# Optimization experiments

Measured on AMD Instinct MI355X. Metric: run time of the kernel, lower is better.

Reference implementation:

```python
import jax, jax.numpy as jnp
import numpy as np

N = 50000      # nodes
E = 800000     # edges
IN = 256       # in_dim
D = 64         # hidden_dim per head
H = 4          # heads
OUT = 40       # out_dim (classes)
SLOPE = 0.2    # leaky relu negative slope


def _gat_conv(h, src, dst, W, al, ar, heads, dh, res=None, act=False):
    """DGL-style GATConv. h:[N,Fin], W:[Fin,heads*dh], al/ar:[heads,dh]."""
    n = h.shape[0]
    feat = (h @ W).reshape(n, heads, dh)                 # [N,H,D]
    el = jnp.sum(feat * al, axis=-1)                     # [N,H]
    er = jnp.sum(feat * ar, axis=-1)                     # [N,H]
    e = jax.nn.leaky_relu(el[src] + er[dst], SLOPE)      # [E,H]
    # segment softmax over incoming edges of each dst node
    m = jax.ops.segment_max(e, dst, num_segments=n)      # [N,H]
    ex = jnp.exp(e - m[dst])                             # [E,H]
    s = jax.ops.segment_sum(ex, dst, num_segments=n)     # [N,H]
    alpha = ex / s[dst]                                  # [E,H]
    rst = jax.ops.segment_sum(alpha[:, :, None] * feat[src], dst, num_segments=n)  # [N,H,D]
    if res is not None:
        rst = rst + res
    if act:
        rst = jax.nn.elu(rst)
    return rst


def setup_inputs():
    key = jax.random.key(0)
    ks = jax.random.split(key, 16)
    def p(k, shape, fan_in):
        return (jax.random.normal(k, shape, jnp.float32) / np.sqrt(fan_in)).astype(jnp.float32)
    inputs = jax.random.normal(ks[0], (N, IN), jnp.float32)
    src = jax.random.randint(ks[1], (E,), 0, N, dtype=jnp.int32)
    dst = jax.random.randint(ks[2], (E,), 0, N, dtype=jnp.int32)
    return {
        "inputs": inputs, "src": src, "dst": dst,
        "W0": p(ks[3], (IN, H * D), IN), "al0": p(ks[4], (H, D), D), "ar0": p(ks[5], (H, D), D),
        "W1": p(ks[6], (H * D, H * D), H * D), "al1": p(ks[7], (H, D), D), "ar1": p(ks[8], (H, D), D),
        "Wo": p(ks[9], (H * D, H * OUT), H * D), "alo": p(ks[10], (H, OUT), OUT), "aro": p(ks[11], (H, OUT), OUT),
        "res_Wo": p(ks[12], (H * D, H * OUT), H * D),
        "fc_W": p(ks[13], (IN, D), IN),
    }


def reference(inputs, src, dst, W0, al0, ar0, W1, al1, ar1, Wo, alo, aro, res_Wo, fc_W):
    # layer 0: no residual, elu activation
    h = _gat_conv(inputs, src, dst, W0, al0, ar0, H, D, res=None, act=True)
    h = h.reshape(N, H * D)
    # layer 1: identity residual (in_feats == heads*out_feats), elu
    res1 = h.reshape(N, H, D)
    h = _gat_conv(h, src, dst, W1, al1, ar1, H, D, res=res1, act=True)
    h = h.reshape(N, H * D)
    # output layer: linear residual projection, no activation, mean over heads
    res_o = (h @ res_Wo).reshape(N, H, OUT)
    logits = _gat_conv(h, src, dst, Wo, alo, aro, H, OUT, res=res_o, act=False).mean(axis=1)
    seq_fts = inputs @ fc_W
    return (logits, h, seq_fts)
```

## Files before the change

### kernel.cpp

```cpp
#include <hip/hip_runtime.h>

typedef unsigned short u16;
typedef unsigned int u32;
typedef __attribute__((ext_vector_type(8))) short short8;
typedef __attribute__((ext_vector_type(4))) float f32x4;

#define NN 50000
#define EE 800000

__device__ __forceinline__ float b2f(u16 u){ union{float f;u32 i;}x; x.i=((u32)u)<<16; return x.f; }
__device__ __forceinline__ u16 f2b(float f){ union{float f;u32 i;}x; x.f=f; u32 i=x.i; return (u16)((i + 0x7fffu + ((i>>16)&1u))>>16); }

__global__ void k_f2b4(const float* __restrict__ x, u16* __restrict__ y, int n4){
  int i = blockIdx.x*256 + threadIdx.x;
  if (i >= n4) return;
  float4 v = ((const float4*)x)[i];
  ushort4 o; o.x=f2b(v.x); o.y=f2b(v.y); o.z=f2b(v.z); o.w=f2b(v.w);
  ((ushort4*)y)[i]=o;
}

__global__ void k_catWo(const float* __restrict__ rWo, const float* __restrict__ Wo, u16* __restrict__ Bcat){
  int i = blockIdx.x*256 + threadIdx.x;
  if (i >= 256*320) return;
  int k = i/320, c = i%320;
  float v = (c < 160) ? rWo[k*160 + c] : Wo[k*160 + (c-160)];
  Bcat[i] = f2b(v);
}

__global__ void k_count(const int* __restrict__ dst, int* __restrict__ cnt){
  int i = blockIdx.x*256+threadIdx.x; if (i<EE) atomicAdd(&cnt[dst[i]],1);
}

__global__ void k_scan_blocks(const int* __restrict__ cnt, int* __restrict__ off, int* __restrict__ part, int n){
  __shared__ int ts[256];
  int t = threadIdx.x; int base = blockIdx.x*1024 + t*4;
  int c0 = (base+0<n)?cnt[base+0]:0;
  int c1 = (base+1<n)?cnt[base+1]:0;
  int c2 = (base+2<n)?cnt[base+2]:0;
  int c3 = (base+3<n)?cnt[base+3]:0;
  int s = c0+c1+c2+c3;
  ts[t]=s; __syncthreads();
  for (int d=1; d<256; d<<=1){ int v=(t>=d)?ts[t-d]:0; __syncthreads(); ts[t]+=v; __syncthreads(); }
  int ex = ts[t]-s;
  if (t==255) part[blockIdx.x]=ts[255];
  if (base+0<n) off[base+0]=ex; ex+=c0;
  if (base+1<n) off[base+1]=ex; ex+=c1;
  if (base+2<n) off[base+2]=ex; ex+=c2;
  if (base+3<n) off[base+3]=ex;
}

__global__ void k_scan_part(int* part, int nb){
  if (threadIdx.x==0 && blockIdx.x==0){ int run=0; for(int i=0;i<nb;++i){ int v=part[i]; part[i]=run; run+=v; } }
}

__global__ void k_addback(int* off, const int* __restrict__ part, int n){
  int base = blockIdx.x*1024 + threadIdx.x*4; int p = part[blockIdx.x];
  #pragma unroll
  for (int j=0;j<4;++j) if (base+j<n) off[base+j]+=p;
}

__global__ void k_copy(const int* __restrict__ a, int* __restrict__ b, int n){
  int i=blockIdx.x*256+threadIdx.x; if(i<n) b[i]=a[i];
}

__global__ void k_scatter(const int* __restrict__ src, const int* __restrict__ dst, int* __restrict__ cur,
                          int* __restrict__ srcs){
  int i = blockIdx.x*256+threadIdx.x; if (i>=EE) return;
  int d = dst[i]; int p = atomicAdd(&cur[d],1);
  srcs[p]=src[i];
}

template<int MODE>
__global__ __launch_bounds__(256) void k_gemm(const u16* __restrict__ A, const u16* __restrict__ B,
                                              void* __restrict__ C0, void* __restrict__ C1,
                                              int M, int N){
  __shared__ u16 Bt[64][266];
  const int tid = threadIdx.x;
  const int n0 = blockIdx.y * 64;
  const int row0 = blockIdx.x * 256;
  #pragma unroll
  for (int r=0; r<32; ++r){
    int lin = r*256 + tid;
    int kk = lin >> 5;
    int cp = (lin & 31) << 1;
    ushort2 v = *(const ushort2*)(B + (size_t)kk*N + n0 + cp);
    Bt[cp][kk] = v.x; Bt[cp+1][kk] = v.y;
  }
  __syncthreads();
  const int w = tid >> 6, l = tid & 63;
  const int lr = l & 15, lq = l >> 4;
  const int wrow = row0 + w*64;
  f32x4 acc[4][4];
  #pragma unroll
  for (int fr=0; fr<4; ++fr)
    #pragma unroll
    for (int j=0; j<4; ++j) acc[fr][j] = (f32x4)0.0f;
  #pragma unroll
  for (int k0 = 0; k0 < 256; k0 += 32){
    short8 a[4], b[4];
    #pragma unroll
    for (int fr=0; fr<4; ++fr){
      int r = wrow + fr*16 + lr; r = r < M ? r : M-1;
      a[fr] = *(const short8*)(A + (size_t)r*256 + k0 + lq*8);
    }
    #pragma unroll
    for (int j=0; j<4; ++j)
      b[j] = *(const short8*)(&Bt[j*16 + lr][k0 + lq*8]);
    #pragma unroll
    for (int fr=0; fr<4; ++fr)
      #pragma unroll
      for (int j=0; j<4; ++j)
        acc[fr][j] = __builtin_amdgcn_mfma_f32_16x16x32_bf16(a[fr], b[j], acc[fr][j], 0, 0, 0);
  }
  #pragma unroll
  for (int fr=0; fr<4; ++fr)
    #pragma unroll
    for (int j=0; j<4; ++j)
      #pragma unroll
      for (int q=0; q<4; ++q){
        int r = wrow + fr*16 + lq*4 + q;
        if (r < M){
          int c = n0 + j*16 + lr;
          float v = acc[fr][j][q];
          if constexpr (MODE == 0)      ((float*)C0)[(size_t)r*N + c] = v;
          else if constexpr (MODE == 1) ((u16*)C0)[(size_t)r*N + c] = f2b(v);
          else {
            if (c < 160) ((u16*)C0)[(size_t)r*160 + c]       = f2b(v);
            else         ((u16*)C1)[(size_t)r*160 + (c-160)] = f2b(v);
          }
        }
      }
}

__global__ void k_eler(const u16* __restrict__ feat, const float* __restrict__ al, const float* __restrict__ ar,
                       float* __restrict__ el, float* __restrict__ er, int Dh, int HD){
  int t = blockIdx.x*256 + threadIdx.x;
  int n = t >> 6; int l = t & 63;
  if (n >= NN) return;
  int h = l >> 4, s = l & 15;
  const u16* fr = feat + (size_t)n*HD + h*Dh;
  const float* alh = al + h*Dh; const float* arh = ar + h*Dh;
  float accl = 0.f, accr = 0.f;
  for (int d = s; d < Dh; d += 16){ float f = b2f(fr[d]); accl += f*alh[d]; accr += f*arh[d]; }
  #pragma unroll
  for (int m = 8; m >= 1; m >>= 1){ accl += __shfl_xor(accl, m, 64); accr += __shfl_xor(accr, m, 64); }
  if (s == 0){ el[n*4+h] = accl; er[n*4+h] = accr; }
}

__global__ void k_soft(const float* __restrict__ el, const float* __restrict__ er,
                       const int* __restrict__ srcs, const int* __restrict__ off,
                       float* __restrict__ es, float* __restrict__ recs){
  int n = blockIdx.x*256 + threadIdx.x; if (n >= NN) return;
  int o0 = off[n], o1 = off[n+1];
  float4 e4 = ((const float4*)er)[n];
  float4 m; m.x=m.y=m.z=m.w=-1e30f;
  for (int i=o0;i<o1;++i){
    float4 a = ((const float4*)el)[srcs[i]];
    float vx=a.x+e4.x; vx = vx>=0.f?vx:0.2f*vx;
    float vy=a.y+e4.y; vy = vy>=0.f?vy:0.2f*vy;
    float vz=a.z+e4.z; vz = vz>=0.f?vz:0.2f*vz;
    float vw=a.w+e4.w; vw = vw>=0.f?vw:0.2f*vw;
    m.x=fmaxf(m.x,vx); m.y=fmaxf(m.y,vy); m.z=fmaxf(m.z,vz); m.w=fmaxf(m.w,vw);
  }
  float4 s; s.x=s.y=s.z=s.w=0.f;
  for (int i=o0;i<o1;++i){
    float4 a = ((const float4*)el)[srcs[i]];
    float vx=a.x+e4.x; vx = vx>=0.f?vx:0.2f*vx;
    float vy=a.y+e4.y; vy = vy>=0.f?vy:0.2f*vy;
    float vz=a.z+e4.z; vz = vz>=0.f?vz:0.2f*vz;
    float vw=a.w+e4.w; vw = vw>=0.f?vw:0.2f*vw;
    float4 v;
    v.x=__expf(vx-m.x); v.y=__expf(vy-m.y); v.z=__expf(vz-m.z); v.w=__expf(vw-m.w);
    ((float4*)es)[i]=v; s.x+=v.x; s.y+=v.y; s.z+=v.z; s.w+=v.w;
  }
  float4 r;
  r.x = s.x>0.f ? 1.f/s.x : 0.f;
  r.y = s.y>0.f ? 1.f/s.y : 0.f;
  r.z = s.z>0.f ? 1.f/s.z : 0.f;
  r.w = s.w>0.f ? 1.f/s.w : 0.f;
  ((float4*)recs)[n] = r;
}

template<bool RES>
__global__ __launch_bounds__(256) void k_agg64(const u16* __restrict__ feat, const float* __restrict__ es,
    const float* __restrict__ recs, const int* __restrict__ off, const int* __restrict__ srcs,
    const u16* __restrict__ resid, float* __restrict__ outf, u16* __restrict__ outb){
  int l = threadIdx.x & 63, w = threadIdx.x >> 6;
  int n = blockIdx.x*4 + w;
  int o0 = off[n], o1 = off[n+1];
  int h = l >> 4;
  float ax=0.f, ay=0.f, az=0.f, aw=0.f;
  int i = o0;
  for (; i + 4 <= o1; i += 4){
    int s0 = srcs[i], s1 = srcs[i+1], s2 = srcs[i+2], s3 = srcs[i+3];
    float e0 = es[(size_t)i*4 + h],     e1 = es[(size_t)(i+1)*4 + h];
    float e2 = es[(size_t)(i+2)*4 + h], e3 = es[(size_t)(i+3)*4 + h];
    ushort4 f0 = *(const ushort4*)(feat + (size_t)s0*256 + l*4);
    ushort4 f1 = *(const ushort4*)(feat + (size_t)s1*256 + l*4);
    ushort4 f2 = *(const ushort4*)(feat + (size_t)s2*256 + l*4);
    ushort4 f3 = *(const ushort4*)(feat + (size_t)s3*256 + l*4);
    ax += e0*b2f(f0.x) + e1*b2f(f1.x) + e2*b2f(f2.x) + e3*b2f(f3.x);
    ay += e0*b2f(f0.y) + e1*b2f(f1.y) + e2*b2f(f2.y) + e3*b2f(f3.y);
    az += e0*b2f(f0.z) + e1*b2f(f1.z) + e2*b2f(f2.z) + e3*b2f(f3.z);
    aw += e0*b2f(f0.w) + e1*b2f(f1.w) + e2*b2f(f2.w) + e3*b2f(f3.w);
  }
  for (; i < o1; ++i){
    int s0 = srcs[i];
    float e0 = es[(size_t)i*4 + h];
    ushort4 f0 = *(const ushort4*)(feat + (size_t)s0*256 + l*4);
    ax += e0*b2f(f0.x); ay += e0*b2f(f0.y); az += e0*b2f(f0.z); aw += e0*b2f(f0.w);
  }
  float rc = recs[n*4+h];
  float vx = ax*rc, vy = ay*rc, vz = az*rc, vw = aw*rc;
  if (RES){
    ushort4 r4 = *(const ushort4*)(resid + (size_t)n*256 + l*4);
    vx += b2f(r4.x); vy += b2f(r4.y); vz += b2f(r4.z); vw += b2f(r4.w);
  }
  vx = vx > 0.f ? vx : expm1f(vx);
  vy = vy > 0.f ? vy : expm1f(vy);
  vz = vz > 0.f ? vz : expm1f(vz);
  vw = vw > 0.f ? vw : expm1f(vw);
  if (outf){ float4 v; v.x=vx; v.y=vy; v.z=vz; v.w=vw; *(float4*)(outf + (size_t)n*256 + l*4) = v; }
  ushort4 ob; ob.x=f2b(vx); ob.y=f2b(vy); ob.z=f2b(vz); ob.w=f2b(vw);
  *(ushort4*)(outb + (size_t)n*256 + l*4) = ob;
}

__global__ __launch_bounds__(256) void k_agg_out(const u16* __restrict__ feat, const float* __restrict__ es,
    const float* __restrict__ recs, const int* __restrict__ off, const int* __restrict__ srcs,
    const u16* __restrict__ reso, float* __restrict__ logits){
  __shared__ float2 red[4][4][80];
  __shared__ float fin[4][160];
  const int l = threadIdx.x & 63, w = threadIdx.x >> 6;
  const int n = blockIdx.x*4 + w;
  const int o0 = off[n], o1 = off[n+1];
  int sArr[5], dpArr[5], hArr[5];
  #pragma unroll
  for (int r=0;r<5;++r){
    int p = r*64 + l;
    sArr[r] = p/80; dpArr[r] = p%80; hArr[r] = dpArr[r]/20;
  }
  float2 acc[5];
  #pragma unroll
  for (int r=0;r<5;++r){ acc[r].x=0.f; acc[r].y=0.f; }
  for (int i0 = o0; i0 < o1; i0 += 4){
    int cnt = o1 - i0;
    #pragma unroll
    for (int r=0;r<5;++r){
      int s = sArr[r];
      bool valid = s < cnt;
      int e = valid ? (i0 + s) : i0;
      int sv = srcs[e];
      float al = es[(size_t)e*4 + hArr[r]];
      ushort2 f = *(const ushort2*)(feat + (size_t)sv*160 + dpArr[r]*2);
      if (!valid) al = 0.f;
      acc[r].x += al * b2f(f.x);
      acc[r].y += al * b2f(f.y);
    }
  }
  #pragma unroll
  for (int r=0;r<5;++r) red[w][sArr[r]][dpArr[r]] = acc[r];
  __syncthreads();
  float4 rc = ((const float4*)recs)[n];
  const float* rcp = (const float*)&rc;
  {
    int dp = l;
    float vx = red[w][0][dp].x + red[w][1][dp].x + red[w][2][dp].x + red[w][3][dp].x;
    float vy = red[w][0][dp].y + red[w][1][dp].y + red[w][2][dp].y + red[w][3][dp].y;
    float r0 = rcp[dp/20];
    ushort2 rr = *(const ushort2*)(reso + (size_t)n*160 + dp*2);
    fin[w][dp*2]   = vx*r0 + b2f(rr.x);
    fin[w][dp*2+1] = vy*r0 + b2f(rr.y);
  }
  if (l < 16){
    int dp = 64 + l;
    float vx = red[w][0][dp].x + red[w][1][dp].x + red[w][2][dp].x + red[w][3][dp].x;
    float vy = red[w][0][dp].y + red[w][1][dp].y + red[w][2][dp].y + red[w][3][dp].y;
    float r0 = rcp[3];
    ushort2 rr = *(const ushort2*)(reso + (size_t)n*160 + dp*2);
    fin[w][dp*2]   = vx*r0 + b2f(rr.x);
    fin[w][dp*2+1] = vy*r0 + b2f(rr.y);
  }
  __syncthreads();
  if (l < 40) logits[(size_t)n*40 + l] = 0.25f*(fin[w][l]+fin[w][l+40]+fin[w][l+80]+fin[w][l+120]);
}

extern "C" void kernel_launch(void* const* d_in, const int* in_sizes, int n_in,
                              void* d_out, int out_size, void* d_ws, size_t ws_size,
                              hipStream_t stream){
  const float* inputs = (const float*)d_in[0];
  const int*   src    = (const int*)d_in[1];
  const int*   dst    = (const int*)d_in[2];
  const float* W0  = (const float*)d_in[3];
  const float* al0 = (const float*)d_in[4];
  const float* ar0 = (const float*)d_in[5];
  const float* W1  = (const float*)d_in[6];
  const float* al1 = (const float*)d_in[7];
  const float* ar1 = (const float*)d_in[8];
  const float* Wo  = (const float*)d_in[9];
  const float* alo = (const float*)d_in[10];
  const float* aro = (const float*)d_in[11];
  const float* rWo = (const float*)d_in[12];
  const float* fcW = (const float*)d_in[13];

  float* out = (float*)d_out;
  float* out_logits = out;
  float* out_h      = out + 2000000;
  float* out_seq    = out + 14800000;

  char* ws = (char*)d_ws;
  size_t o = 0;
  auto alc = [&](size_t bytes){ size_t r = o; o += (bytes + 255) & ~(size_t)255; return r; };
  size_t oXb   = alc((size_t)NN*256*2);
  size_t oFA   = alc((size_t)NN*256*2);
  size_t oFB   = alc((size_t)NN*256*2);
  size_t oEs   = alc((size_t)EE*4*4);
  size_t oSrcs = alc((size_t)EE*4);
  size_t oOff  = alc((size_t)(NN+1)*4);
  size_t oCnt  = alc((size_t)(NN+1)*4);
  size_t oCur  = alc((size_t)NN*4);
  size_t oPart = alc(64*4);
  size_t oEl   = alc((size_t)NN*4*4);
  size_t oEr   = alc((size_t)NN*4*4);
  size_t oRecs = alc((size_t)NN*4*4);
  size_t oReso = alc((size_t)NN*160*2);
  size_t oW0b  = alc(256*256*2);
  size_t oW1b  = alc(256*256*2);
  size_t oWcat = alc(256*320*2);
  size_t oFcb  = alc(256*64*2);
  if (ws_size < o) return;

  u16* Xb   = (u16*)(ws + oXb);
  u16* fA   = (u16*)(ws + oFA);
  u16* fB   = (u16*)(ws + oFB);
  float* es = (float*)(ws + oEs);
  int* srcs = (int*)(ws + oSrcs);
  int* off  = (int*)(ws + oOff);
  int* cnt  = (int*)(ws + oCnt);
  int* cur  = (int*)(ws + oCur);
  int* part = (int*)(ws + oPart);
  float* el = (float*)(ws + oEl);
  float* er = (float*)(ws + oEr);
  float* recs = (float*)(ws + oRecs);
  u16* reso = (u16*)(ws + oReso);
  u16* W0b  = (u16*)(ws + oW0b);
  u16* W1b  = (u16*)(ws + oW1b);
  u16* Wcat = (u16*)(ws + oWcat);
  u16* fcb  = (u16*)(ws + oFcb);

  k_f2b4<<<(NN*256/4 + 255)/256, 256, 0, stream>>>(inputs, Xb, NN*256/4);
  k_f2b4<<<(65536/4 + 255)/256, 256, 0, stream>>>(W0, W0b, 65536/4);
  k_f2b4<<<(65536/4 + 255)/256, 256, 0, stream>>>(W1, W1b, 65536/4);
  k_catWo<<<(256*320 + 255)/256, 256, 0, stream>>>(rWo, Wo, Wcat);
  k_f2b4<<<(16384/4 + 255)/256, 256, 0, stream>>>(fcW, fcb, 16384/4);

  hipMemsetAsync(cnt, 0, (size_t)(NN+1)*4, stream);
  k_count<<<(EE+255)/256, 256, 0, stream>>>(dst, cnt);
  const int NP1 = NN+1, NB = (NP1 + 1023)/1024;
  k_scan_blocks<<<NB, 256, 0, stream>>>(cnt, off, part, NP1);
  k_scan_part<<<1, 64, 0, stream>>>(part, NB);
  k_addback<<<NB, 256, 0, stream>>>(off, part, NP1);
  k_copy<<<(NN+255)/256, 256, 0, stream>>>(off, cur, NN);
  k_scatter<<<(EE+255)/256, 256, 0, stream>>>(src, dst, cur, srcs);

  dim3 gN256((NN+255)/256, 4), gN320((NN+255)/256, 5), gN64((NN+255)/256, 1);

  k_gemm<0><<<gN64, 256, 0, stream>>>(Xb, fcb, out_seq, nullptr, NN, 64);

  k_gemm<1><<<gN256, 256, 0, stream>>>(Xb, W0b, fA, nullptr, NN, 256);
  k_eler<<<(NN*64 + 255)/256, 256, 0, stream>>>(fA, al0, ar0, el, er, 64, 256);
  k_soft<<<(NN+255)/256, 256, 0, stream>>>(el, er, srcs, off, es, recs);
  k_agg64<false><<<NN/4, 256, 0, stream>>>(fA, es, recs, off, srcs, nullptr, nullptr, fB);

  k_gemm<1><<<gN256, 256, 0, stream>>>(fB, W1b, fA, nullptr, NN, 256);
  k_eler<<<(NN*64 + 255)/256, 256, 0, stream>>>(fA, al1, ar1, el, er, 64, 256);
  k_soft<<<(NN+255)/256, 256, 0, stream>>>(el, er, srcs, off, es, recs);
  k_agg64<true><<<NN/4, 256, 0, stream>>>(fA, es, recs, off, srcs, fB, out_h, fB);

  k_gemm<2><<<gN320, 256, 0, stream>>>(fB, Wcat, reso, fA, NN, 320);
  k_eler<<<(NN*64 + 255)/256, 256, 0, stream>>>(fA, alo, aro, el, er, 40, 160);
  k_soft<<<(NN+255)/256, 256, 0, stream>>>(el, er, srcs, off, es, recs);
  k_agg_out<<<NN/4, 256, 0, stream>>>(fA, es, recs, off, srcs, reso, out_logits);
}
```

Baseline: 566.5 us.

## Widen gather loads in aggregation kernels and cache leaky-relu scores in softmax

The 64-dim aggregation now has each half-wavefront handle a different edge, with 16-byte bf16 loads per lane, and combines the two halves with a cross-lane shuffle. The output-layer aggregation switches to 8-byte loads and 8 edges per iteration, reducing through a larger shared-memory buffer. The softmax kernel stores the leaky-relu scores during the max pass and rereads them, so it no longer gathers el[src] a second time. A specialized el/er kernel for 256-wide features uses vectorized loads of features and attention weights. Risks are extra writes to es, idle half-wavefronts during the epilogue, and tail-edge masking overhead on low-degree nodes.

```diff
diff --git a/kernel.cpp b/kernel.cpp
--- a/kernel.cpp
+++ b/kernel.cpp
@@ -132,6 +132,23 @@
       }
 }
 
+__global__ void k_eler256(const u16* __restrict__ feat, const float* __restrict__ al, const float* __restrict__ ar,
+                          float* __restrict__ el, float* __restrict__ er){
+  int t = blockIdx.x*256 + threadIdx.x;
+  int n = t >> 6, l = t & 63;
+  if (n >= NN) return;
+  float4 a4 = ((const float4*)al)[l];
+  float4 r4 = ((const float4*)ar)[l];
+  ushort4 f = *(const ushort4*)(feat + (size_t)n*256 + l*4);
+  float f0=b2f(f.x), f1=b2f(f.y), f2=b2f(f.z), f3=b2f(f.w);
+  float accl = f0*a4.x + f1*a4.y + f2*a4.z + f3*a4.w;
+  float accr = f0*r4.x + f1*r4.y + f2*r4.z + f3*r4.w;
+  #pragma unroll
+  for (int m = 8; m >= 1; m >>= 1){ accl += __shfl_xor(accl, m, 64); accr += __shfl_xor(accr, m, 64); }
+  int h = l >> 4;
+  if ((l & 15) == 0){ el[n*4+h] = accl; er[n*4+h] = accr; }
+}
+
 __global__ void k_eler(const u16* __restrict__ feat, const float* __restrict__ al, const float* __restrict__ ar,
                        float* __restrict__ el, float* __restrict__ er, int Dh, int HD){
   int t = blockIdx.x*256 + threadIdx.x;
@@ -156,21 +173,18 @@
   float4 m; m.x=m.y=m.z=m.w=-1e30f;
   for (int i=o0;i<o1;++i){
     float4 a = ((const float4*)el)[srcs[i]];
-    float vx=a.x+e4.x; vx = vx>=0.f?vx:0.2f*vx;
-    float vy=a.y+e4.y; vy = vy>=0.f?vy:0.2f*vy;
-    float vz=a.z+e4.z; vz = vz>=0.f?vz:0.2f*vz;
-    float vw=a.w+e4.w; vw = vw>=0.f?vw:0.2f*vw;
-    m.x=fmaxf(m.x,vx); m.y=fmaxf(m.y,vy); m.z=fmaxf(m.z,vz); m.w=fmaxf(m.w,vw);
+    float4 v;
+    v.x=a.x+e4.x; v.x = v.x>=0.f?v.x:0.2f*v.x;
+    v.y=a.y+e4.y; v.y = v.y>=0.f?v.y:0.2f*v.y;
+    v.z=a.z+e4.z; v.z = v.z>=0.f?v.z:0.2f*v.z;
+    v.w=a.w+e4.w; v.w = v.w>=0.f?v.w:0.2f*v.w;
+    ((float4*)es)[i]=v;
+    m.x=fmaxf(m.x,v.x); m.y=fmaxf(m.y,v.y); m.z=fmaxf(m.z,v.z); m.w=fmaxf(m.w,v.w);
   }
   float4 s; s.x=s.y=s.z=s.w=0.f;
   for (int i=o0;i<o1;++i){
-    float4 a = ((const float4*)el)[srcs[i]];
-    float vx=a.x+e4.x; vx = vx>=0.f?vx:0.2f*vx;
-    float vy=a.y+e4.y; vy = vy>=0.f?vy:0.2f*vy;
-    float vz=a.z+e4.z; vz = vz>=0.f?vz:0.2f*vz;
-    float vw=a.w+e4.w; vw = vw>=0.f?vw:0.2f*vw;
-    float4 v;
-    v.x=__expf(vx-m.x); v.y=__expf(vy-m.y); v.z=__expf(vz-m.z); v.w=__expf(vw-m.w);
+    float4 v = ((const float4*)es)[i];
+    v.x=__expf(v.x-m.x); v.y=__expf(v.y-m.y); v.z=__expf(v.z-m.z); v.w=__expf(v.w-m.w);
     ((float4*)es)[i]=v; s.x+=v.x; s.y+=v.y; s.z+=v.z; s.w+=v.w;
   }
   float4 r;
@@ -185,100 +199,113 @@
 __global__ __launch_bounds__(256) void k_agg64(const u16* __restrict__ feat, const float* __restrict__ es,
     const float* __restrict__ recs, const int* __restrict__ off, const int* __restrict__ srcs,
     const u16* __restrict__ resid, float* __restrict__ outf, u16* __restrict__ outb){
-  int l = threadIdx.x & 63, w = threadIdx.x >> 6;
-  int n = blockIdx.x*4 + w;
-  int o0 = off[n], o1 = off[n+1];
-  int h = l >> 4;
-  float ax=0.f, ay=0.f, az=0.f, aw=0.f;
+  const int l = threadIdx.x & 63, w = threadIdx.x >> 6;
+  const int n = blockIdx.x*4 + w;
+  const int o0 = off[n], o1 = off[n+1];
+  const int lh = l & 31;
+  const int half = l >> 5;
+  const int h = lh >> 3;
+  float a0=0.f,a1=0.f,a2=0.f,a3=0.f,a4=0.f,a5=0.f,a6=0.f,a7=0.f;
   int i = o0;
-  for (; i + 4 <= o1; i += 4){
-    int s0 = srcs[i], s1 = srcs[i+1], s2 = srcs[i+2], s3 = srcs[i+3];
-    float e0 = es[(size_t)i*4 + h],     e1 = es[(size_t)(i+1)*4 + h];
-    float e2 = es[(size_t)(i+2)*4 + h], e3 = es[(size_t)(i+3)*4 + h];
-    ushort4 f0 = *(const ushort4*)(feat + (size_t)s0*256 + l*4);
-    ushort4 f1 = *(const ushort4*)(feat + (size_t)s1*256 + l*4);
-    ushort4 f2 = *(const ushort4*)(feat + (size_t)s2*256 + l*4);
-    ushort4 f3 = *(const ushort4*)(feat + (size_t)s3*256 + l*4);
-    ax += e0*b2f(f0.x) + e1*b2f(f1.x) + e2*b2f(f2.x) + e3*b2f(f3.x);
-    ay += e0*b2f(f0.y) + e1*b2f(f1.y) + e2*b2f(f2.y) + e3*b2f(f3.y);
-    az += e0*b2f(f0.z) + e1*b2f(f1.z) + e2*b2f(f2.z) + e3*b2f(f3.z);
-    aw += e0*b2f(f0.w) + e1*b2f(f1.w) + e2*b2f(f2.w) + e3*b2f(f3.w);
-  }
-  for (; i < o1; ++i){
-    int s0 = srcs[i];
-    float e0 = es[(size_t)i*4 + h];
-    ushort4 f0 = *(const ushort4*)(feat + (size_t)s0*256 + l*4);
-    ax += e0*b2f(f0.x); ay += e0*b2f(f0.y); az += e0*b2f(f0.z); aw += e0*b2f(f0.w);
-  }
-  float rc = recs[n*4+h];
-  float vx = ax*rc, vy = ay*rc, vz = az*rc, vw = aw*rc;
-  if (RES){
-    ushort4 r4 = *(const ushort4*)(resid + (size_t)n*256 + l*4);
-    vx += b2f(r4.x); vy += b2f(r4.y); vz += b2f(r4.z); vw += b2f(r4.w);
-  }
-  vx = vx > 0.f ? vx : expm1f(vx);
-  vy = vy > 0.f ? vy : expm1f(vy);
-  vz = vz > 0.f ? vz : expm1f(vz);
-  vw = vw > 0.f ? vw : expm1f(vw);
-  if (outf){ float4 v; v.x=vx; v.y=vy; v.z=vz; v.w=vw; *(float4*)(outf + (size_t)n*256 + l*4) = v; }
-  ushort4 ob; ob.x=f2b(vx); ob.y=f2b(vy); ob.z=f2b(vz); ob.w=f2b(vw);
-  *(ushort4*)(outb + (size_t)n*256 + l*4) = ob;
+  for (; i + 8 <= o1; i += 8){
+    #pragma unroll
+    for (int u=0; u<4; ++u){
+      int e = i + u*2 + half;
+      int sv = srcs[e];
+      float al = es[(size_t)e*4 + h];
+      short8 f = *(const short8*)(feat + (size_t)sv*256 + lh*8);
+      a0 += al*b2f((u16)f[0]); a1 += al*b2f((u16)f[1]);
+      a2 += al*b2f((u16)f[2]); a3 += al*b2f((u16)f[3]);
+      a4 += al*b2f((u16)f[4]); a5 += al*b2f((u16)f[5]);
+      a6 += al*b2f((u16)f[6]); a7 += al*b2f((u16)f[7]);
+    }
+  }
+  for (; i < o1; i += 2){
+    int e = i + half;
+    bool valid = e < o1;
+    int ec = valid ? e : i;
+    int sv = srcs[ec];
+    float al = valid ? es[(size_t)ec*4 + h] : 0.f;
+    short8 f = *(const short8*)(feat + (size_t)sv*256 + lh*8);
+    a0 += al*b2f((u16)f[0]); a1 += al*b2f((u16)f[1]);
+    a2 += al*b2f((u16)f[2]); a3 += al*b2f((u16)f[3]);
+    a4 += al*b2f((u16)f[4]); a5 += al*b2f((u16)f[5]);
+    a6 += al*b2f((u16)f[6]); a7 += al*b2f((u16)f[7]);
+  }
+  a0 += __shfl_xor(a0,32,64); a1 += __shfl_xor(a1,32,64);
+  a2 += __shfl_xor(a2,32,64); a3 += __shfl_xor(a3,32,64);
+  a4 += __shfl_xor(a4,32,64); a5 += __shfl_xor(a5,32,64);
+  a6 += __shfl_xor(a6,32,64); a7 += __shfl_xor(a7,32,64);
+  if (half == 0){
+    float rc = recs[n*4+h];
+    float v[8] = {a0*rc,a1*rc,a2*rc,a3*rc,a4*rc,a5*rc,a6*rc,a7*rc};
+    if (RES){
+      short8 r8 = *(const short8*)(resid + (size_t)n*256 + lh*8);
+      #pragma unroll
+      for (int j=0;j<8;++j) v[j] += b2f((u16)r8[j]);
+    }
+    #pragma unroll
+    for (int j=0;j<8;++j) v[j] = v[j] > 0.f ? v[j] : expm1f(v[j]);
+    if (outf){
+      float4 q0; q0.x=v[0]; q0.y=v[1]; q0.z=v[2]; q0.w=v[3];
+      float4 q1; q1.x=v[4]; q1.y=v[5]; q1.z=v[6]; q1.w=v[7];
+      *(float4*)(outf + (size_t)n*256 + lh*8)     = q0;
+      *(float4*)(outf + (size_t)n*256 + lh*8 + 4) = q1;
+    }
+    short8 ob;
+    #pragma unroll
+    for (int j=0;j<8;++j) ob[j] = (short)f2b(v[j]);
+    *(short8*)(outb + (size_t)n*256 + lh*8) = ob;
+  }
 }
 
 __global__ __launch_bounds__(256) void k_agg_out(const u16* __restrict__ feat, const float* __restrict__ es,
     const float* __restrict__ recs, const int* __restrict__ off, const int* __restrict__ srcs,
     const u16* __restrict__ reso, float* __restrict__ logits){
-  __shared__ float2 red[4][4][80];
+  __shared__ f32x4 red[4][8][40];
   __shared__ float fin[4][160];
   const int l = threadIdx.x & 63, w = threadIdx.x >> 6;
   const int n = blockIdx.x*4 + w;
   const int o0 = off[n], o1 = off[n+1];
-  int sArr[5], dpArr[5], hArr[5];
+  int sA[5], qA[5], hA[5];
   #pragma unroll
   for (int r=0;r<5;++r){
     int p = r*64 + l;
-    sArr[r] = p/80; dpArr[r] = p%80; hArr[r] = dpArr[r]/20;
-  }
-  float2 acc[5];
-  #pragma unroll
-  for (int r=0;r<5;++r){ acc[r].x=0.f; acc[r].y=0.f; }
-  for (int i0 = o0; i0 < o1; i0 += 4){
+    sA[r] = p/40; qA[r] = p%40; hA[r] = qA[r]/10;
+  }
+  f32x4 acc[5];
+  #pragma unroll
+  for (int r=0;r<5;++r) acc[r] = (f32x4)0.0f;
+  for (int i0 = o0; i0 < o1; i0 += 8){
     int cnt = o1 - i0;
     #pragma unroll
     for (int r=0;r<5;++r){
-      int s = sArr[r];
+      int s = sA[r];
       bool valid = s < cnt;
       int e = valid ? (i0 + s) : i0;
       int sv = srcs[e];
-      float al = es[(size_t)e*4 + hArr[r]];
-      ushort2 f = *(const ushort2*)(feat + (size_t)sv*160 + dpArr[r]*2);
+      float al = es[(size_t)e*4 + hA[r]];
+      ushort4 f = *(const ushort4*)(feat + (size_t)sv*160 + qA[r]*4);
       if (!valid) al = 0.f;
-      acc[r].x += al * b2f(f.x);
-      acc[r].y += al * b2f(f.y);
+      acc[r][0] += al*b2f(f.x); acc[r][1] += al*b2f(f.y);
+      acc[r][2] += al*b2f(f.z); acc[r][3] += al*b2f(f.w);
     }
   }
   #pragma unroll
-  for (int r=0;r<5;++r) red[w][sArr[r]][dpArr[r]] = acc[r];
+  for (int r=0;r<5;++r) red[w][sA[r]][qA[r]] = acc[r];
   __syncthreads();
-  float4 rc = ((const float4*)recs)[n];
-  const float* rcp = (const float*)&rc;
-  {
-    int dp = l;
-    float vx = red[w][0][dp].x + red[w][1][dp].x + red[w][2][dp].x + red[w][3][dp].x;
-    float vy = red[w][0][dp].y + red[w][1][dp].y + red[w][2][dp].y + red[w][3][dp].y;
-    float r0 = rcp[dp/20];
-    ushort2 rr = *(const ushort2*)(reso + (size_t)n*160 + dp*2);
-    fin[w][dp*2]   = vx*r0 + b2f(rr.x);
-    fin[w][dp*2+1] = vy*r0 + b2f(rr.y);
-  }
-  if (l < 16){
-    int dp = 64 + l;
-    float vx = red[w][0][dp].x + red[w][1][dp].x + red[w][2][dp].x + red[w][3][dp].x;
-    float vy = red[w][0][dp].y + red[w][1][dp].y + red[w][2][dp].y + red[w][3][dp].y;
-    float r0 = rcp[3];
-    ushort2 rr = *(const ushort2*)(reso + (size_t)n*160 + dp*2);
-    fin[w][dp*2]   = vx*r0 + b2f(rr.x);
-    fin[w][dp*2+1] = vy*r0 + b2f(rr.y);
+  if (l < 40){
+    f32x4 v = red[w][0][l];
+    #pragma unroll
+    for (int s=1;s<8;++s) v += red[w][s][l];
+    float4 rc = ((const float4*)recs)[n];
+    const float* rcp = (const float*)&rc;
+    float rch = rcp[l/10];
+    ushort4 rr = *(const ushort4*)(reso + (size_t)n*160 + l*4);
+    fin[w][l*4+0] = v[0]*rch + b2f(rr.x);
+    fin[w][l*4+1] = v[1]*rch + b2f(rr.y);
+    fin[w][l*4+2] = v[2]*rch + b2f(rr.z);
+    fin[w][l*4+3] = v[3]*rch + b2f(rr.w);
   }
   __syncthreads();
   if (l < 40) logits[(size_t)n*40 + l] = 0.25f*(fin[w][l]+fin[w][l+40]+fin[w][l+80]+fin[w][l+120]);
@@ -367,12 +394,12 @@
   k_gemm<0><<<gN64, 256, 0, stream>>>(Xb, fcb, out_seq, nullptr, NN, 64);
 
   k_gemm<1><<<gN256, 256, 0, stream>>>(Xb, W0b, fA, nullptr, NN, 256);
-  k_eler<<<(NN*64 + 255)/256, 256, 0, stream>>>(fA, al0, ar0, el, er, 64, 256);
+  k_eler256<<<(NN*64 + 255)/256, 256, 0, stream>>>(fA, al0, ar0, el, er);
   k_soft<<<(NN+255)/256, 256, 0, stream>>>(el, er, srcs, off, es, recs);
   k_agg64<false><<<NN/4, 256, 0, stream>>>(fA, es, recs, off, srcs, nullptr, nullptr, fB);
 
   k_gemm<1><<<gN256, 256, 0, stream>>>(fB, W1b, fA, nullptr, NN, 256);
-  k_eler<<<(NN*64 + 255)/256, 256, 0, stream>>>(fA, al1, ar1, el, er, 64, 256);
+  k_eler256<<<(NN*64 + 255)/256, 256, 0, stream>>>(fA, al1, ar1, el, er);
   k_soft<<<(NN+255)/256, 256, 0, stream>>>(el, er, srcs, off, es, recs);
   k_agg64<true><<<NN/4, 256, 0, stream>>>(fA, es, recs, off, srcs, fB, out_h, fB);
 
```

After: 586.9 us. 3.6% more time.
